# Optimization experiments

Hardware: AMD Instinct MI355X
Metric: run time of the kernel (lower is better)

The kernel has to match this reference:

```python
import jax, jax.numpy as jnp
import numpy as np

# ---- st-moe constants (training-mode routing) ----
EPS = 1e-9
TOP_N = 2
CAP_FACTOR = 1.25      # capacity_factor_train
THRESHOLD = 0.2        # threshold_train (2nd expert)
BAL_COEF = 0.01
Z_COEF = 0.001
MIN_CAP = 4
LN_EPS = 1e-5

B, N, D, E = 4, 2048, 512, 8
H = int(D * 4 * 2 / 3)  # 1365, st-moe default Expert hidden


def _rms_norm(x, gamma):
    # F.normalize(x, dim=-1) * sqrt(d) * gamma
    nrm = jnp.maximum(jnp.linalg.norm(x, axis=-1, keepdims=True), 1e-12)
    return x / nrm * (x.shape[-1] ** 0.5) * gamma


def setup_inputs() -> dict:
    key = jax.random.key(0)
    ks = jax.random.split(key, 6)
    s = 0.02
    return {
        "x": jax.random.normal(ks[0], (B, N, D), jnp.float32),
        "gate_w": jax.random.normal(ks[1], (D, E), jnp.float32) * s,
        "prenorm_g": jnp.ones((D,), jnp.float32),
        "w1": jax.random.normal(ks[2], (E, D, 2 * H), jnp.float32) * s,
        "b1": jnp.zeros((E, 2 * H), jnp.float32),
        "mult_bias": jnp.ones((E, H), jnp.float32),
        "w2": jax.random.normal(ks[3], (E, H, D), jnp.float32) * s,
        "b2": jnp.zeros((E, D), jnp.float32),
        "ln_g": jnp.ones((D,), jnp.float32),
        "ln_b": jnp.zeros((D,), jnp.float32),
    }


def _stmoe_fnn(x, gate_w, prenorm_g, w1, b1, mult_bias, w2, b2, ln_g, ln_b):
    b, n, d = x.shape
    e = gate_w.shape[1]
    cap = max(MIN_CAP, min(n, int(n * CAP_FACTOR / e)))  # static python int

    # SparseMoEBlock: moe(RMSNorm(x)) + x
    xg = _rms_norm(x, prenorm_g)

    # ---- TopNGating ----
    gate_logits = jnp.einsum('bnd,de->bne', xg, gate_w)
    raw_gates = jax.nn.softmax(gate_logits, axis=-1)
    gates, idx = jax.lax.top_k(raw_gates, TOP_N)          # (b,n,k)
    gates = jnp.moveaxis(gates, -1, 0)                    # (k,b,n)
    idx = jnp.moveaxis(idx, -1, 0)                        # (k,b,n)
    one_hot = jax.nn.one_hot(idx, e, dtype=x.dtype)       # (k,b,n,e)

    denom = jnp.maximum(gates.sum(axis=0), EPS)
    gates = gates / denom                                 # normalized top-n scores

    # stochastic routing to non-first experts: prob = min(1, gate/threshold)
    thresh = jnp.array([EPS, THRESHOLD], x.dtype)[:, None, None]
    probs = jax.random.uniform(jax.random.key(42), gates.shape, x.dtype)
    should_route = probs < (gates / jnp.maximum(thresh, EPS))
    should_route = should_route.at[0].set(True)
    mask = one_hot * should_route[..., None].astype(x.dtype)  # (k,b,n,e)

    # exclusive cumsum over sequence -> position within each expert
    mask_cumsum = jnp.cumsum(mask, axis=-2) - mask

    positions, kept_masks = [], []
    prev_count = jnp.zeros((b, 1, e), x.dtype)
    for k in range(TOP_N):  # top_n=2, tiny static loop
        pos_in_expert = (mask_cumsum[k] + prev_count) * mask[k]      # (b,n,e)
        kept = mask[k] * (pos_in_expert < float(cap)).astype(x.dtype)
        prev_count = prev_count + kept.sum(axis=-2, keepdims=True)
        positions.append(pos_in_expert.sum(axis=-1))                 # (b,n)
        kept_masks.append(kept)
    mask = jnp.stack(kept_masks)       # (k,b,n,e) post-capacity
    positions = jnp.stack(positions)   # (k,b,n)

    mask_flat = mask.sum(axis=-1)      # (k,b,n)
    gates = gates * mask_flat

    # safe one-hot: out-of-range (overflow) positions map to all-zeros
    pos_one_hot = jax.nn.one_hot(positions.astype(jnp.int32), cap, dtype=x.dtype)  # (k,b,n,c)
    combine = jnp.einsum('kbn,kbne,kbnc->bnec', gates, one_hot, pos_one_hot)       # (b,n,e,c)

    # straight-through dispatch tensor
    dispatch = (combine > 0).astype(x.dtype) + combine - jax.lax.stop_gradient(combine)

    # ---- dispatch, expert GEGLU FFN, combine ----
    expert_in = jnp.einsum('bnd,bnec->becd', xg, dispatch)                 # (b,e,c,d)
    h = jnp.einsum('becd,edf->becf', expert_in, w1) + b1[None, :, None, :]
    u, g = jnp.split(h, 2, axis=-1)
    act = u * jax.nn.gelu(g, approximate=False) * mult_bias[None, :, None, :]
    expert_out = jnp.einsum('bech,ehd->becd', act, w2) + b2[None, :, None, :]
    moe_out = jnp.einsum('becd,bnec->bnd', expert_out, combine)

    # ---- aux losses (training mode) ----
    density_1 = mask[0].mean(axis=-2)          # (b,e), post-capacity mask (torch in-place view)
    density_proxy = raw_gates.mean(axis=-2)    # (b,e)
    balance_loss = (density_proxy * density_1).mean() * float(e ** 2)
    z = jax.nn.logsumexp(gate_logits, axis=-1)
    router_z_loss = jnp.mean(z * z)
    total_aux = BAL_COEF * balance_loss + Z_COEF * router_z_loss

    # residual, (dropout -> identity for determinism), LayerNorm
    y = moe_out + x
    mu = y.mean(axis=-1, keepdims=True)
    var = jnp.mean((y - mu) ** 2, axis=-1, keepdims=True)
    out = (y - mu) * jax.lax.rsqrt(var + LN_EPS) * ln_g + ln_b
    return out, total_aux


def reference(x, gate_w, prenorm_g, w1, b1, mult_bias, w2, b2, ln_g, ln_b):
    return _stmoe_fnn(x, gate_w, prenorm_g, w1, b1, mult_bias, w2, b2, ln_g, ln_b)
```

## Files before the change

kernel.cpp:

```cpp
#include <hip/hip_runtime.h>
#include <hip/hip_bf16.h>
#include <math.h>

#define BB 4
#define NN 2048
#define DD 512
#define EE 8
#define HH 1365
#define H2 2730
#define CAP 320
#define NT (BB*NN)
#define KP2 1408
#define NW1 2816
#define ME 1280
#define KS1 16
#define KS2 44

typedef __bf16 bf16_t;
typedef __bf16 bf16x4 __attribute__((ext_vector_type(4)));
typedef __bf16 bf16x8 __attribute__((ext_vector_type(8)));
typedef float f32x4 __attribute__((ext_vector_type(4)));

__device__ __forceinline__ float gelu_exact(float x){
    return 0.5f * x * (1.0f + erff(x * 0.70710678118654752f));
}
__device__ __forceinline__ void gl2lds16(const void* g, void* s){
    __builtin_amdgcn_global_load_lds((const __attribute__((address_space(1))) unsigned int*)g,
                                     (__attribute__((address_space(3))) unsigned int*)s,
                                     16, 0, 0);
}
__device__ __forceinline__ unsigned rotl32(unsigned x, int d){ return (x<<d)|(x>>(32-d)); }
__device__ __forceinline__ void tf_round(unsigned &x0, unsigned &x1, int r){
    x0 += x1; x1 = rotl32(x1, r); x1 ^= x0;
}
__device__ float threefry_u01_second(unsigned t){
    const unsigned ks0 = 0u, ks1 = 42u, ks2 = 0x1BD11BDAu ^ 42u;
    unsigned x0 = t, x1 = t + 8192u;
    x0 += ks0; x1 += ks1;
    tf_round(x0,x1,13); tf_round(x0,x1,15); tf_round(x0,x1,26); tf_round(x0,x1,6);
    x0 += ks1; x1 += ks2 + 1u;
    tf_round(x0,x1,17); tf_round(x0,x1,29); tf_round(x0,x1,16); tf_round(x0,x1,24);
    x0 += ks2; x1 += ks0 + 2u;
    tf_round(x0,x1,13); tf_round(x0,x1,15); tf_round(x0,x1,26); tf_round(x0,x1,6);
    x0 += ks0; x1 += ks1 + 3u;
    tf_round(x0,x1,17); tf_round(x0,x1,29); tf_round(x0,x1,16); tf_round(x0,x1,24);
    x0 += ks1; x1 += ks2 + 4u;
    tf_round(x0,x1,13); tf_round(x0,x1,15); tf_round(x0,x1,26); tf_round(x0,x1,6);
    x0 += ks2; x1 += ks0 + 5u;
    unsigned bits = (x1 >> 9) | 0x3f800000u;
    return __uint_as_float(bits) - 1.0f;
}

__global__ void k_gate(const float* __restrict__ x, const float* __restrict__ png,
                       const float* __restrict__ gw, bf16_t* __restrict__ xgb,
                       int* __restrict__ tok_e0, int* __restrict__ tok_e1,
                       float* __restrict__ tok_g0, float* __restrict__ tok_g1,
                       int* __restrict__ tok_c0, int* __restrict__ tok_c1,
                       float* __restrict__ dpPart, float* __restrict__ z2Part){
    if (blockIdx.x == NN){
        xgb[(size_t)NT*DD + threadIdx.x]       = (bf16_t)0.f;
        xgb[(size_t)NT*DD + threadIdx.x + 256] = (bf16_t)0.f;
        return;
    }
    int wave = threadIdx.x >> 6;
    int lane = threadIdx.x & 63;
    int t = blockIdx.x*4 + wave;
    const float* row = x + (size_t)t*DD;
    float xv[8]; float ss = 0.f;
    #pragma unroll
    for (int i=0;i<8;i++){ xv[i] = row[lane + i*64]; ss += xv[i]*xv[i]; }
    #pragma unroll
    for (int off=32; off; off>>=1) ss += __shfl_xor(ss, off);
    float scale = 22.62741699796952f / fmaxf(sqrtf(ss), 1e-12f);
    float acc[EE];
    #pragma unroll
    for (int e=0;e<EE;e++) acc[e]=0.f;
    #pragma unroll
    for (int i=0;i<8;i++){
        int k = lane + i*64;
        float v = xv[i] * scale * png[k];
        xgb[(size_t)t*DD + k] = (bf16_t)v;
        const float* w = gw + k*EE;
        #pragma unroll
        for (int e=0;e<EE;e++) acc[e] = fmaf(v, w[e], acc[e]);
    }
    #pragma unroll
    for (int off=32; off; off>>=1){
        #pragma unroll
        for (int e=0;e<EE;e++) acc[e] += __shfl_down(acc[e], off);
    }
    __shared__ float s_raw[4][EE];
    __shared__ float s_z2[4];
    if (lane==0){
        float mx = acc[0];
        #pragma unroll
        for (int e=1;e<EE;e++) mx = fmaxf(mx, acc[e]);
        float p[EE]; float se=0.f;
        #pragma unroll
        for (int e=0;e<EE;e++){ p[e] = expf(acc[e]-mx); se += p[e]; }
        float inv = 1.f/se;
        #pragma unroll
        for (int e=0;e<EE;e++) p[e] *= inv;
        float z = mx + logf(se);
        int i0=0;
        #pragma unroll
        for (int e=1;e<EE;e++) if (p[e] > p[i0]) i0=e;
        int i1 = (i0==0)?1:0;
        #pragma unroll
        for (int e=0;e<EE;e++){ if (e==i0) continue; if (p[e] > p[i1]) i1=e; }
        float g0=p[i0], g1=p[i1];
        float denom = fmaxf(g0+g1, 1e-9f);
        g0/=denom; g1/=denom;
        float prob = threefry_u01_second((unsigned)t);
        bool route1 = prob < (g1 * 5.0f);
        tok_e0[t] = i0;
        tok_e1[t] = route1 ? i1 : -1;
        tok_g0[t] = g0;
        tok_g1[t] = g1;
        tok_c0[t] = -1;
        tok_c1[t] = -1;
        #pragma unroll
        for (int e=0;e<EE;e++) s_raw[wave][e] = p[e];
        s_z2[wave] = z*z;
    }
    __syncthreads();
    if (threadIdx.x < EE){
        float sum = s_raw[0][threadIdx.x]+s_raw[1][threadIdx.x]+s_raw[2][threadIdx.x]+s_raw[3][threadIdx.x];
        dpPart[threadIdx.x*(size_t)NN + blockIdx.x] = sum;
    }
    if (threadIdx.x == EE) z2Part[blockIdx.x] = s_z2[0]+s_z2[1]+s_z2[2]+s_z2[3];
}

__global__ void k_scan(const int* __restrict__ tok_e0, const int* __restrict__ tok_e1,
                       int* __restrict__ tok_c0, int* __restrict__ tok_c1,
                       int* __restrict__ slot_tok, int* __restrict__ kept0cnt){
    int be = blockIdx.x;
    int b = be >> 3, e = be & 7;
    int tid = threadIdx.x;
    int sbase = (e*BB + b)*CAP;
    for (int i=tid; i<CAP; i+=256) slot_tok[sbase + i] = -1;
    __syncthreads();
    int n0 = tid * 8;
    int base_t = b*NN;
    int m0=0, m1=0;
    for (int i=0;i<8;i++){
        int t = base_t + n0 + i;
        m0 += (tok_e0[t]==e);
        m1 += (tok_e1[t]==e);
    }
    __shared__ int s[256];
    s[tid] = m0 | (m1<<16);
    __syncthreads();
    for (int off=1; off<256; off<<=1){
        int v = 0;
        if (tid >= off) v = s[tid-off];
        __syncthreads();
        if (tid >= off) s[tid] += v;
        __syncthreads();
    }
    int incl = s[tid];
    int total = s[255];
    int p0 = (incl & 0xffff) - m0;
    int p1 = (incl >> 16) - m1;
    int t0 = total & 0xffff;
    int kept0 = min(t0, CAP);
    int c0 = p0, c1 = p1;
    for (int i=0;i<8;i++){
        int n = n0 + i;
        int t = base_t + n;
        if (tok_e0[t]==e){
            int pos = c0++;
            if (pos < CAP){ tok_c0[t] = pos; slot_tok[sbase + pos] = t; }
        }
        if (tok_e1[t]==e){
            int pos = kept0 + c1++;
            if (pos < CAP){ tok_c1[t] = pos; slot_tok[sbase + pos] = t; }
        }
    }
    if (tid==0) kept0cnt[be] = kept0;
}

__global__ void k_aux(const float* __restrict__ dpPart, const float* __restrict__ z2Part,
                      const int* __restrict__ kept0cnt, float* __restrict__ out_aux){
    __shared__ float sdp[32][9];
    __shared__ float sz[256];
    int tid = threadIdx.x;
    float za = 0.f;
    for (int i=tid; i<NN; i+=256) za += z2Part[i];
    sz[tid] = za; __syncthreads();
    for (int off=128; off; off>>=1){ if (tid<off) sz[tid]+=sz[tid+off]; __syncthreads(); }
    int seg = tid >> 3, off8 = tid & 7;
    int b = seg >> 3, e = seg & 7;
    float a = 0.f;
    for (int j=off8; j<512; j+=8) a += dpPart[e*(size_t)NN + b*512 + j];
    sdp[seg][off8] = a;
    __syncthreads();
    if (tid == 0){
        float z2t = sz[0];
        float bal = 0.f;
        for (int sgi=0; sgi<32; sgi++){
            float d = 0.f;
            #pragma unroll
            for (int k=0;k<8;k++) d += sdp[sgi][k];
            float d1 = (float)kept0cnt[sgi] / (float)NN;
            bal += (d / (float)NN) * d1;
        }
        bal = bal / 32.f * 64.f;
        out_aux[0] = 0.01f * bal + 0.001f * (z2t / (float)NT);
    }
}

__global__ void k_w1t(const float* __restrict__ w1, bf16_t* __restrict__ w1t){
    __shared__ float T[32][33];
    int n0 = blockIdx.x * 32;
    int ks = blockIdx.y;
    int e  = blockIdx.z;
    int tx = threadIdx.x & 31;
    int tg = threadIdx.x >> 5;
    int n = n0 + tx;
    #pragma unroll
    for (int i=0;i<4;i++){
        int kk = tg + i*8;
        int k = ks*32 + kk;
        float v = 0.f;
        if (n < KP2){ if (n < HH) v = w1[((size_t)e*DD + k)*H2 + n]; }
        else { int h = n - KP2; if (h < HH) v = w1[((size_t)e*DD + k)*H2 + HH + h]; }
        T[kk][tx] = v;
    }
    __syncthreads();
    int rr = threadIdx.x >> 3, s = threadIdx.x & 7;
    bf16x4 o;
    #pragma unroll
    for (int j=0;j<4;j++) o[j] = (bf16_t)T[s*4+j][rr];
    size_t off = (((size_t)e*KS1 + ks)*NW1 + n0 + rr)*32 + s*4;
    *(bf16x4*)(w1t + off) = o;
}

__global__ void k_w2t(const float* __restrict__ w2, bf16_t* __restrict__ w2t){
    __shared__ float T[32][33];
    int n0 = blockIdx.x * 32;
    int ks = blockIdx.y;
    int e  = blockIdx.z;
    int tx = threadIdx.x & 31;
    int tg = threadIdx.x >> 5;
    #pragma unroll
    for (int i=0;i<4;i++){
        int kk = tg + i*8;
        int k = ks*32 + kk;
        float v = 0.f;
        if (k < HH) v = w2[((size_t)e*HH + k)*DD + n0 + tx];
        T[kk][tx] = v;
    }
    __syncthreads();
    int rr = threadIdx.x >> 3, s = threadIdx.x & 7;
    bf16x4 o;
    #pragma unroll
    for (int j=0;j<4;j++) o[j] = (bf16_t)T[s*4+j][rr];
    size_t off = (((size_t)e*KS2 + ks)*DD + n0 + rr)*32 + s*4;
    *(bf16x4*)(w2t + off) = o;
}

__global__ __launch_bounds__(256,2) void k_ffn1_mfma(
    const bf16_t* __restrict__ xgb, const bf16_t* __restrict__ w1t,
    const float* __restrict__ b1, const float* __restrict__ mbias,
    const int* __restrict__ slot_tok, bf16_t* __restrict__ actb)
{
    int bid = blockIdx.x;
    int e = bid & 7;
    int r = bid >> 3;
    int mblk = r % 10, hb = r / 10;
    int lane = threadIdx.x & 63, wave = threadIdx.x >> 6;
    int quad = lane >> 4, col = lane & 15;
    int wx = wave & 1, wy = wave >> 1;

    __shared__ __align__(16) bf16_t sA[8*512];
    __shared__ __align__(16) bf16_t sB[16*512];

    const bf16_t* gsrc[6];
    bf16_t* sdst[6];
    int gstep[6];
    const size_t w1t_e = (size_t)e*KS1*NW1*32;
    #pragma unroll
    for (int i=0;i<6;i++){
        int id = wave + 4*i;
        if (id < 8){
            int m = mblk*128 + id*16 + col;
            int slot = slot_tok[e*ME + m];
            int row = (slot >= 0) ? slot : NT;
            gsrc[i] = xgb + (size_t)row*DD + quad*8;
            sdst[i] = sA + id*512;
            gstep[i] = 32;
        } else if (id < 16){
            int n = hb*128 + (id-8)*16 + col;
            gsrc[i] = w1t + w1t_e + (size_t)n*32 + quad*8;
            sdst[i] = sB + (id-8)*512;
            gstep[i] = NW1*32;
        } else {
            int n = KP2 + hb*128 + (id-16)*16 + col;
            gsrc[i] = w1t + w1t_e + (size_t)n*32 + quad*8;
            sdst[i] = sB + (id-8)*512;
            gstep[i] = NW1*32;
        }
    }

    f32x4 accU[4][4], accG[4][4];
    #pragma unroll
    for (int mi=0;mi<4;mi++)
        #pragma unroll
        for (int ni=0;ni<4;ni++){
            accU[mi][ni] = (f32x4){0.f,0.f,0.f,0.f};
            accG[mi][ni] = (f32x4){0.f,0.f,0.f,0.f};
        }

    for (int ks=0; ks<KS1; ks++){
        #pragma unroll
        for (int i=0;i<6;i++){ gl2lds16(gsrc[i], sdst[i]); gsrc[i] += gstep[i]; }
        __syncthreads();
        bf16x8 a[4], bu[4], bg[4];
        #pragma unroll
        for (int mi=0;mi<4;mi++) a[mi] = *(const bf16x8*)(sA + (wx*4+mi)*512 + lane*8);
        #pragma unroll
        for (int ni=0;ni<4;ni++){
            bu[ni] = *(const bf16x8*)(sB + (wy*4+ni)*512 + lane*8);
            bg[ni] = *(const bf16x8*)(sB + (8+wy*4+ni)*512 + lane*8);
        }
        #pragma unroll
        for (int mi=0;mi<4;mi++)
            #pragma unroll
            for (int ni=0;ni<4;ni++){
                accU[mi][ni] = __builtin_amdgcn_mfma_f32_16x16x32_bf16(a[mi], bu[ni], accU[mi][ni], 0,0,0);
                accG[mi][ni] = __builtin_amdgcn_mfma_f32_16x16x32_bf16(a[mi], bg[ni], accG[mi][ni], 0,0,0);
            }
        __syncthreads();
    }

    const size_t actb_e = (size_t)e*KS2*ME*32;
    #pragma unroll
    for (int ni=0; ni<4; ni++){
        int h = hb*128 + wy*64 + ni*16 + col;
        bool valid = (h < HH);
        float bu_ = valid ? b1[e*H2 + h] : 0.f;
        float bg_ = valid ? b1[e*H2 + HH + h] : 0.f;
        float mb_ = valid ? mbias[e*HH + h] : 0.f;
        int ks2 = h >> 5, kl = h & 31;
        #pragma unroll
        for (int mi=0; mi<4; mi++){
            int m = mblk*128 + wx*64 + mi*16 + quad*4;
            bf16_t* base = actb + actb_e + ((size_t)ks2*ME + m)*32 + kl;
            #pragma unroll
            for (int rr=0; rr<4; rr++){
                float v = 0.f;
                if (valid){
                    float u = accU[mi][ni][rr] + bu_;
                    float g = accG[mi][ni][rr] + bg_;
                    v = u * gelu_exact(g) * mb_;
                }
                base[rr*32] = (bf16_t)v;
            }
        }
    }
}

__global__ __launch_bounds__(256,4) void k_ffn2_mfma(
    const bf16_t* __restrict__ actb, const bf16_t* __restrict__ w2t,
    const float* __restrict__ b2, float* __restrict__ eo)
{
    int bid = blockIdx.x;
    int e = bid & 7;
    int r = bid >> 3;
    int mblk = r % 10, db = r / 10;
    int lane = threadIdx.x & 63, wave = threadIdx.x >> 6;
    int quad = lane >> 4, col = lane & 15;
    int wx = wave & 1, wy = wave >> 1;

    __shared__ __align__(16) bf16_t sA[8*512];
    __shared__ __align__(16) bf16_t sB[8*512];

    const bf16_t* gsrc[4];
    bf16_t* sdst[4];
    int gstep[4];
    const size_t actb_e = (size_t)e*KS2*ME*32;
    const size_t w2t_e  = (size_t)e*KS2*DD*32;
    #pragma unroll
    for (int i=0;i<4;i++){
        int id = wave + 4*i;
        if (id < 8){
            int m = mblk*128 + id*16 + col;
            gsrc[i] = actb + actb_e + (size_t)m*32 + quad*8;
            sdst[i] = sA + id*512;
            gstep[i] = ME*32;
        } else {
            int d = db*128 + (id-8)*16 + col;
            gsrc[i] = w2t + w2t_e + (size_t)d*32 + quad*8;
            sdst[i] = sB + (id-8)*512;
            gstep[i] = DD*32;
        }
    }

    f32x4 acc[4][4];
    #pragma unroll
    for (int mi=0;mi<4;mi++)
        #pragma unroll
        for (int ni=0;ni<4;ni++) acc[mi][ni] = (f32x4){0.f,0.f,0.f,0.f};

    for (int ks=0; ks<KS2; ks++){
        #pragma unroll
        for (int i=0;i<4;i++){ gl2lds16(gsrc[i], sdst[i]); gsrc[i] += gstep[i]; }
        __syncthreads();
        bf16x8 a[4], bv[4];
        #pragma unroll
        for (int mi=0;mi<4;mi++) a[mi] = *(const bf16x8*)(sA + (wx*4+mi)*512 + lane*8);
        #pragma unroll
        for (int ni=0;ni<4;ni++) bv[ni] = *(const bf16x8*)(sB + (wy*4+ni)*512 + lane*8);
        #pragma unroll
        for (int mi=0;mi<4;mi++)
            #pragma unroll
            for (int ni=0;ni<4;ni++)
                acc[mi][ni] = __builtin_amdgcn_mfma_f32_16x16x32_bf16(a[mi], bv[ni], acc[mi][ni], 0,0,0);
        __syncthreads();
    }

    #pragma unroll
    for (int ni=0; ni<4; ni++){
        int d = db*128 + wy*64 + ni*16 + col;
        float bb = b2[e*DD + d];
        #pragma unroll
        for (int mi=0; mi<4; mi++){
            int m = mblk*128 + wx*64 + mi*16 + quad*4;
            #pragma unroll
            for (int rr=0; rr<4; rr++)
                eo[((size_t)e*ME + m + rr)*DD + d] = acc[mi][ni][rr] + bb;
        }
    }
}

__global__ void k_combine(const float* __restrict__ x, const float* __restrict__ eo,
        const int* __restrict__ tok_e0, const int* __restrict__ tok_e1,
        const int* __restrict__ tok_c0, const int* __restrict__ tok_c1,
        const float* __restrict__ tok_g0, const float* __restrict__ tok_g1,
        const float* __restrict__ ln_g, const float* __restrict__ ln_b,
        float* __restrict__ out){
    int t = blockIdx.x;
    int b = t / NN;
    int e0 = tok_e0[t], c0 = tok_c0[t];
    int e1 = tok_e1[t], c1 = tok_c1[t];
    float g0 = tok_g0[t], g1 = tok_g1[t];
    const float* r0 = (c0>=0) ? eo + ((size_t)(e0*ME + b*CAP + c0))*DD : nullptr;
    const float* r1 = (e1>=0 && c1>=0) ? eo + ((size_t)(e1*ME + b*CAP + c1))*DD : nullptr;
    float y[2]; float s=0.f, s2=0.f;
    #pragma unroll
    for (int i=0;i<2;i++){
        int d = threadIdx.x + i*256;
        float v = x[(size_t)t*DD + d];
        if (r0) v = fmaf(g0, r0[d], v);
        if (r1) v = fmaf(g1, r1[d], v);
        y[i]=v; s+=v; s2+=v*v;
    }
    __shared__ float rs[4], rs2[4];
    #pragma unroll
    for (int off=32; off; off>>=1){ s+=__shfl_down(s,off); s2+=__shfl_down(s2,off); }
    if ((threadIdx.x&63)==0){ rs[threadIdx.x>>6]=s; rs2[threadIdx.x>>6]=s2; }
    __syncthreads();
    float mu  = (rs[0]+rs[1]+rs[2]+rs[3]) * (1.0f/512.0f);
    float var = (rs2[0]+rs2[1]+rs2[2]+rs2[3]) * (1.0f/512.0f) - mu*mu;
    float inv = rsqrtf(var + 1e-5f);
    #pragma unroll
    for (int i=0;i<2;i++){
        int d = threadIdx.x + i*256;
        out[(size_t)t*DD + d] = (y[i]-mu)*inv*ln_g[d] + ln_b[d];
    }
}

extern "C" void kernel_launch(void* const* d_in, const int* in_sizes, int n_in,
                              void* d_out, int out_size, void* d_ws, size_t ws_size,
                              hipStream_t stream) {
    const float* x         = (const float*)d_in[0];
    const float* gate_w    = (const float*)d_in[1];
    const float* prenorm_g = (const float*)d_in[2];
    const float* w1        = (const float*)d_in[3];
    const float* b1        = (const float*)d_in[4];
    const float* mult_bias = (const float*)d_in[5];
    const float* w2        = (const float*)d_in[6];
    const float* b2        = (const float*)d_in[7];
    const float* ln_g      = (const float*)d_in[8];
    const float* ln_b      = (const float*)d_in[9];
    float* out = (float*)d_out;

    char* p = (char*)d_ws;
    bf16_t* xgb = (bf16_t*)p; p += (size_t)(NT+1)*DD*2;
    bf16_t* w1t = (bf16_t*)p; p += (size_t)EE*KS1*NW1*32*2;
    bf16_t* w2t = (bf16_t*)p; p += (size_t)EE*KS2*DD*32*2;
    bf16_t* actb = (bf16_t*)p; p += (size_t)EE*KS2*ME*32*2;
    float* eo  = (float*)p; p += (size_t)EE*ME*DD*4;
    int* slot_tok = (int*)p; p += EE*BB*CAP*4;
    int* tok_e0 = (int*)p; p += NT*4;
    int* tok_e1 = (int*)p; p += NT*4;
    int* tok_c0 = (int*)p; p += NT*4;
    int* tok_c1 = (int*)p; p += NT*4;
    float* tok_g0 = (float*)p; p += NT*4;
    float* tok_g1 = (float*)p; p += NT*4;
    float* dpPart = (float*)p; p += EE*NN*4;
    float* z2Part = (float*)p; p += NN*4;
    int* kept0 = (int*)p; p += BB*EE*4;

    k_w1t<<<dim3(NW1/32, KS1, EE), 256, 0, stream>>>(w1, w1t);
    k_w2t<<<dim3(DD/32, KS2, EE), 256, 0, stream>>>(w2, w2t);
    k_gate<<<NN+1, 256, 0, stream>>>(x, prenorm_g, gate_w, xgb,
                                     tok_e0, tok_e1, tok_g0, tok_g1,
                                     tok_c0, tok_c1, dpPart, z2Part);
    k_scan<<<BB*EE, 256, 0, stream>>>(tok_e0, tok_e1, tok_c0, tok_c1, slot_tok, kept0);
    k_aux<<<1, 256, 0, stream>>>(dpPart, z2Part, kept0, out + (size_t)NT*DD);
    k_ffn1_mfma<<<EE*10*11, 256, 0, stream>>>(xgb, w1t, b1, mult_bias, slot_tok, actb);
    k_ffn2_mfma<<<EE*10*4, 256, 0, stream>>>(actb, w2t, b2, eo);
    k_combine<<<NT, 256, 0, stream>>>(x, eo, tok_e0, tok_e1, tok_c0, tok_c1,
                                      tok_g0, tok_g1, ln_g, ln_b, out);
}
```

Baseline: 272.6 us.

## Fuse prep kernels, split-K FFN2 with bf16 partials, retile FFN1, vectorize combine

Merges the weight transposes and gating into a single prep launch and folds the aux-loss reduction into the scan kernel using a last-block atomic counter. FFN1 is retiled to 512-thread blocks covering 256 rows so the weight tile is reused across more tokens. FFN2 is split along K into two halves that write bf16 partial outputs, and the combine kernel sums them, adds the bias and uses float4 loads. This aims to cut launch overhead, raise GEMM parallelism and reduce expert-output traffic, at the cost of lower output precision and an extra partial buffer.

Result: no change. 269.1 us (-1.3%).

```diff
diff --git a/kernel.cpp b/kernel.cpp
--- a/kernel.cpp
+++ b/kernel.cpp
@@ -51,89 +51,152 @@
     return __uint_as_float(bits) - 1.0f;
 }
 
-__global__ void k_gate(const float* __restrict__ x, const float* __restrict__ png,
-                       const float* __restrict__ gw, bf16_t* __restrict__ xgb,
+#define PREP_GATE  2048
+#define PREP_W1    (PREP_GATE+1)
+#define PREP_W2    (PREP_W1+11264)
+__global__ void k_prep(const float* __restrict__ x, const float* __restrict__ png,
+                       const float* __restrict__ gw,
+                       const float* __restrict__ w1, const float* __restrict__ w2,
+                       bf16_t* __restrict__ xgb, bf16_t* __restrict__ w1t, bf16_t* __restrict__ w2t,
                        int* __restrict__ tok_e0, int* __restrict__ tok_e1,
                        float* __restrict__ tok_g0, float* __restrict__ tok_g1,
                        int* __restrict__ tok_c0, int* __restrict__ tok_c1,
-                       float* __restrict__ dpPart, float* __restrict__ z2Part){
-    if (blockIdx.x == NN){
+                       float* __restrict__ dpPart, float* __restrict__ z2Part,
+                       unsigned* __restrict__ scanCnt){
+    __shared__ float T[32][33];
+    __shared__ float s_raw[4][EE];
+    __shared__ float s_z2[4];
+    int bid = blockIdx.x;
+    if (bid < PREP_GATE){
+        int wave = threadIdx.x >> 6;
+        int lane = threadIdx.x & 63;
+        int t = bid*4 + wave;
+        const float* row = x + (size_t)t*DD;
+        float xv[8]; float ss = 0.f;
+        #pragma unroll
+        for (int i=0;i<8;i++){ xv[i] = row[lane + i*64]; ss += xv[i]*xv[i]; }
+        #pragma unroll
+        for (int off=32; off; off>>=1) ss += __shfl_xor(ss, off);
+        float scale = 22.62741699796952f / fmaxf(sqrtf(ss), 1e-12f);
+        float acc[EE];
+        #pragma unroll
+        for (int e=0;e<EE;e++) acc[e]=0.f;
+        #pragma unroll
+        for (int i=0;i<8;i++){
+            int k = lane + i*64;
+            float v = xv[i] * scale * png[k];
+            xgb[(size_t)t*DD + k] = (bf16_t)v;
+            const float* w = gw + k*EE;
+            #pragma unroll
+            for (int e=0;e<EE;e++) acc[e] = fmaf(v, w[e], acc[e]);
+        }
+        #pragma unroll
+        for (int off=32; off; off>>=1){
+            #pragma unroll
+            for (int e=0;e<EE;e++) acc[e] += __shfl_down(acc[e], off);
+        }
+        if (lane==0){
+            float mx = acc[0];
+            #pragma unroll
+            for (int e=1;e<EE;e++) mx = fmaxf(mx, acc[e]);
+            float p[EE]; float se=0.f;
+            #pragma unroll
+            for (int e=0;e<EE;e++){ p[e] = expf(acc[e]-mx); se += p[e]; }
+            float inv = 1.f/se;
+            #pragma unroll
+            for (int e=0;e<EE;e++) p[e] *= inv;
+            float z = mx + logf(se);
+            int i0=0;
+            #pragma unroll
+            for (int e=1;e<EE;e++) if (p[e] > p[i0]) i0=e;
+            int i1 = (i0==0)?1:0;
+            #pragma unroll
+            for (int e=0;e<EE;e++){ if (e==i0) continue; if (p[e] > p[i1]) i1=e; }
+            float g0=p[i0], g1=p[i1];
+            float denom = fmaxf(g0+g1, 1e-9f);
+            g0/=denom; g1/=denom;
+            float prob = threefry_u01_second((unsigned)t);
+            bool route1 = prob < (g1 * 5.0f);
+            tok_e0[t] = i0;
+            tok_e1[t] = route1 ? i1 : -1;
+            tok_g0[t] = g0;
+            tok_g1[t] = g1;
+            tok_c0[t] = -1;
+            tok_c1[t] = -1;
+            #pragma unroll
+            for (int e=0;e<EE;e++) s_raw[wave][e] = p[e];
+            s_z2[wave] = z*z;
+        }
+        __syncthreads();
+        if (threadIdx.x < EE){
+            float sum = s_raw[0][threadIdx.x]+s_raw[1][threadIdx.x]+s_raw[2][threadIdx.x]+s_raw[3][threadIdx.x];
+            dpPart[threadIdx.x*(size_t)NN + bid] = sum;
+        }
+        if (threadIdx.x == EE) z2Part[bid] = s_z2[0]+s_z2[1]+s_z2[2]+s_z2[3];
+    } else if (bid == PREP_GATE){
         xgb[(size_t)NT*DD + threadIdx.x]       = (bf16_t)0.f;
         xgb[(size_t)NT*DD + threadIdx.x + 256] = (bf16_t)0.f;
-        return;
-    }
-    int wave = threadIdx.x >> 6;
-    int lane = threadIdx.x & 63;
-    int t = blockIdx.x*4 + wave;
-    const float* row = x + (size_t)t*DD;
-    float xv[8]; float ss = 0.f;
-    #pragma unroll
-    for (int i=0;i<8;i++){ xv[i] = row[lane + i*64]; ss += xv[i]*xv[i]; }
-    #pragma unroll
-    for (int off=32; off; off>>=1) ss += __shfl_xor(ss, off);
-    float scale = 22.62741699796952f / fmaxf(sqrtf(ss), 1e-12f);
-    float acc[EE];
-    #pragma unroll
-    for (int e=0;e<EE;e++) acc[e]=0.f;
-    #pragma unroll
-    for (int i=0;i<8;i++){
-        int k = lane + i*64;
-        float v = xv[i] * scale * png[k];
-        xgb[(size_t)t*DD + k] = (bf16_t)v;
-        const float* w = gw + k*EE;
-        #pragma unroll
-        for (int e=0;e<EE;e++) acc[e] = fmaf(v, w[e], acc[e]);
-    }
-    #pragma unroll
-    for (int off=32; off; off>>=1){
-        #pragma unroll
-        for (int e=0;e<EE;e++) acc[e] += __shfl_down(acc[e], off);
-    }
-    __shared__ float s_raw[4][EE];
-    __shared__ float s_z2[4];
-    if (lane==0){
-        float mx = acc[0];
-        #pragma unroll
-        for (int e=1;e<EE;e++) mx = fmaxf(mx, acc[e]);
-        float p[EE]; float se=0.f;
-        #pragma unroll
-        for (int e=0;e<EE;e++){ p[e] = expf(acc[e]-mx); se += p[e]; }
-        float inv = 1.f/se;
-        #pragma unroll
-        for (int e=0;e<EE;e++) p[e] *= inv;
-        float z = mx + logf(se);
-        int i0=0;
-        #pragma unroll
-        for (int e=1;e<EE;e++) if (p[e] > p[i0]) i0=e;
-        int i1 = (i0==0)?1:0;
-        #pragma unroll
-        for (int e=0;e<EE;e++){ if (e==i0) continue; if (p[e] > p[i1]) i1=e; }
-        float g0=p[i0], g1=p[i1];
-        float denom = fmaxf(g0+g1, 1e-9f);
-        g0/=denom; g1/=denom;
-        float prob = threefry_u01_second((unsigned)t);
-        bool route1 = prob < (g1 * 5.0f);
-        tok_e0[t] = i0;
-        tok_e1[t] = route1 ? i1 : -1;
-        tok_g0[t] = g0;
-        tok_g1[t] = g1;
-        tok_c0[t] = -1;
-        tok_c1[t] = -1;
-        #pragma unroll
-        for (int e=0;e<EE;e++) s_raw[wave][e] = p[e];
-        s_z2[wave] = z*z;
-    }
-    __syncthreads();
-    if (threadIdx.x < EE){
-        float sum = s_raw[0][threadIdx.x]+s_raw[1][threadIdx.x]+s_raw[2][threadIdx.x]+s_raw[3][threadIdx.x];
-        dpPart[threadIdx.x*(size_t)NN + blockIdx.x] = sum;
-    }
-    if (threadIdx.x == EE) z2Part[blockIdx.x] = s_z2[0]+s_z2[1]+s_z2[2]+s_z2[3];
+        if (threadIdx.x == 0) scanCnt[0] = 0u;
+    } else if (bid < PREP_W2){
+        int f = bid - PREP_W1;
+        int n32 = f % 88;
+        int ks  = (f / 88) % 16;
+        int e   = f / 1408;
+        int n0 = n32 * 32;
+        int tx = threadIdx.x & 31;
+        int tg = threadIdx.x >> 5;
+        int n = n0 + tx;
+        #pragma unroll
+        for (int i=0;i<4;i++){
+            int kk = tg + i*8;
+            int k = ks*32 + kk;
+            float v = 0.f;
+            if (n < KP2){ if (n < HH) v = w1[((size_t)e*DD + k)*H2 + n]; }
+            else { int h = n - KP2; if (h < HH) v = w1[((size_t)e*DD + k)*H2 + HH + h]; }
+            T[kk][tx] = v;
+        }
+        __syncthreads();
+        int rr = threadIdx.x >> 3, s = threadIdx.x & 7;
+        bf16x4 o;
+        #pragma unroll
+        for (int j=0;j<4;j++) o[j] = (bf16_t)T[s*4+j][rr];
+        size_t off = (((size_t)e*KS1 + ks)*NW1 + n0 + rr)*32 + s*4;
+        *(bf16x4*)(w1t + off) = o;
+    } else {
+        int f = bid - PREP_W2;
+        int d32 = f % 16;
+        int ks  = (f / 16) % 44;
+        int e   = f / 704;
+        int n0 = d32 * 32;
+        int tx = threadIdx.x & 31;
+        int tg = threadIdx.x >> 5;
+        #pragma unroll
+        for (int i=0;i<4;i++){
+            int kk = tg + i*8;
+            int k = ks*32 + kk;
+            float v = 0.f;
+            if (k < HH) v = w2[((size_t)e*HH + k)*DD + n0 + tx];
+            T[kk][tx] = v;
+        }
+        __syncthreads();
+        int rr = threadIdx.x >> 3, s = threadIdx.x & 7;
+        bf16x4 o;
+        #pragma unroll
+        for (int j=0;j<4;j++) o[j] = (bf16_t)T[s*4+j][rr];
+        size_t off = (((size_t)e*KS2 + ks)*DD + n0 + rr)*32 + s*4;
+        *(bf16x4*)(w2t + off) = o;
+    }
 }
 
 __global__ void k_scan(const int* __restrict__ tok_e0, const int* __restrict__ tok_e1,
                        int* __restrict__ tok_c0, int* __restrict__ tok_c1,
-                       int* __restrict__ slot_tok, int* __restrict__ kept0cnt){
+                       int* __restrict__ slot_tok, int* __restrict__ kept0cnt,
+                       const float* __restrict__ dpPart, const float* __restrict__ z2Part,
+                       unsigned* __restrict__ scanCnt, float* __restrict__ out_aux){
+    __shared__ int s[256];
+    __shared__ float sdp[32][9];
+    __shared__ float sz[256];
+    __shared__ bool s_last;
     int be = blockIdx.x;
     int b = be >> 3, e = be & 7;
     int tid = threadIdx.x;
@@ -148,7 +211,6 @@
         m0 += (tok_e0[t]==e);
         m1 += (tok_e1[t]==e);
     }
-    __shared__ int s[256];
     s[tid] = m0 | (m1<<16);
     __syncthreads();
     for (int off=1; off<256; off<<=1){
@@ -178,21 +240,23 @@
         }
     }
     if (tid==0) kept0cnt[be] = kept0;
-}
-
-__global__ void k_aux(const float* __restrict__ dpPart, const float* __restrict__ z2Part,
-                      const int* __restrict__ kept0cnt, float* __restrict__ out_aux){
-    __shared__ float sdp[32][9];
-    __shared__ float sz[256];
-    int tid = threadIdx.x;
+    __threadfence();
+    __syncthreads();
+    if (tid==0){
+        unsigned old = atomicAdd(scanCnt, 1u);
+        s_last = (old == (unsigned)(BB*EE - 1));
+    }
+    __syncthreads();
+    if (!s_last) return;
+    __threadfence();
     float za = 0.f;
     for (int i=tid; i<NN; i+=256) za += z2Part[i];
     sz[tid] = za; __syncthreads();
     for (int off=128; off; off>>=1){ if (tid<off) sz[tid]+=sz[tid+off]; __syncthreads(); }
     int seg = tid >> 3, off8 = tid & 7;
-    int b = seg >> 3, e = seg & 7;
+    int bb2 = seg >> 3, ee2 = seg & 7;
     float a = 0.f;
-    for (int j=off8; j<512; j+=8) a += dpPart[e*(size_t)NN + b*512 + j];
+    for (int j=off8; j<512; j+=8) a += dpPart[ee2*(size_t)NN + bb2*512 + j];
     sdp[seg][off8] = a;
     __syncthreads();
     if (tid == 0){
@@ -210,57 +274,7 @@
     }
 }
 
-__global__ void k_w1t(const float* __restrict__ w1, bf16_t* __restrict__ w1t){
-    __shared__ float T[32][33];
-    int n0 = blockIdx.x * 32;
-    int ks = blockIdx.y;
-    int e  = blockIdx.z;
-    int tx = threadIdx.x & 31;
-    int tg = threadIdx.x >> 5;
-    int n = n0 + tx;
-    #pragma unroll
-    for (int i=0;i<4;i++){
-        int kk = tg + i*8;
-        int k = ks*32 + kk;
-        float v = 0.f;
-        if (n < KP2){ if (n < HH) v = w1[((size_t)e*DD + k)*H2 + n]; }
-        else { int h = n - KP2; if (h < HH) v = w1[((size_t)e*DD + k)*H2 + HH + h]; }
-        T[kk][tx] = v;
-    }
-    __syncthreads();
-    int rr = threadIdx.x >> 3, s = threadIdx.x & 7;
-    bf16x4 o;
-    #pragma unroll
-    for (int j=0;j<4;j++) o[j] = (bf16_t)T[s*4+j][rr];
-    size_t off = (((size_t)e*KS1 + ks)*NW1 + n0 + rr)*32 + s*4;
-    *(bf16x4*)(w1t + off) = o;
-}
-
-__global__ void k_w2t(const float* __restrict__ w2, bf16_t* __restrict__ w2t){
-    __shared__ float T[32][33];
-    int n0 = blockIdx.x * 32;
-    int ks = blockIdx.y;
-    int e  = blockIdx.z;
-    int tx = threadIdx.x & 31;
-    int tg = threadIdx.x >> 5;
-    #pragma unroll
-    for (int i=0;i<4;i++){
-        int kk = tg + i*8;
-        int k = ks*32 + kk;
-        float v = 0.f;
-        if (k < HH) v = w2[((size_t)e*HH + k)*DD + n0 + tx];
-        T[kk][tx] = v;
-    }
-    __syncthreads();
-    int rr = threadIdx.x >> 3, s = threadIdx.x & 7;
-    bf16x4 o;
-    #pragma unroll
-    for (int j=0;j<4;j++) o[j] = (bf16_t)T[s*4+j][rr];
-    size_t off = (((size_t)e*KS2 + ks)*DD + n0 + rr)*32 + s*4;
-    *(bf16x4*)(w2t + off) = o;
-}
-
-__global__ __launch_bounds__(256,2) void k_ffn1_mfma(
+__global__ __launch_bounds__(512,2) void k_ffn1_mfma(
     const bf16_t* __restrict__ xgb, const bf16_t* __restrict__ w1t,
     const float* __restrict__ b1, const float* __restrict__ mbias,
     const int* __restrict__ slot_tok, bf16_t* __restrict__ actb)
@@ -268,37 +282,38 @@
     int bid = blockIdx.x;
     int e = bid & 7;
     int r = bid >> 3;
-    int mblk = r % 10, hb = r / 10;
+    int mblk = r % 5, hb = r / 5;
     int lane = threadIdx.x & 63, wave = threadIdx.x >> 6;
     int quad = lane >> 4, col = lane & 15;
-    int wx = wave & 1, wy = wave >> 1;
-
-    __shared__ __align__(16) bf16_t sA[8*512];
-    __shared__ __align__(16) bf16_t sB[16*512];
-
-    const bf16_t* gsrc[6];
-    bf16_t* sdst[6];
-    int gstep[6];
+    int wm = wave & 3, wn = wave >> 2;
+
+    __shared__ __align__(16) bf16_t sA[16*512];
+    __shared__ __align__(16) bf16_t sBu[8*512];
+    __shared__ __align__(16) bf16_t sBg[8*512];
+
+    const bf16_t* gsrc[4];
+    bf16_t* sdst[4];
+    int gstep[4];
     const size_t w1t_e = (size_t)e*KS1*NW1*32;
     #pragma unroll
-    for (int i=0;i<6;i++){
-        int id = wave + 4*i;
-        if (id < 8){
-            int m = mblk*128 + id*16 + col;
+    for (int i=0;i<4;i++){
+        int id = wave + 8*i;
+        if (id < 16){
+            int m = mblk*256 + id*16 + col;
             int slot = slot_tok[e*ME + m];
             int row = (slot >= 0) ? slot : NT;
             gsrc[i] = xgb + (size_t)row*DD + quad*8;
             sdst[i] = sA + id*512;
             gstep[i] = 32;
-        } else if (id < 16){
-            int n = hb*128 + (id-8)*16 + col;
+        } else if (id < 24){
+            int n = hb*128 + (id-16)*16 + col;
             gsrc[i] = w1t + w1t_e + (size_t)n*32 + quad*8;
-            sdst[i] = sB + (id-8)*512;
+            sdst[i] = sBu + (id-16)*512;
             gstep[i] = NW1*32;
         } else {
-            int n = KP2 + hb*128 + (id-16)*16 + col;
+            int n = KP2 + hb*128 + (id-24)*16 + col;
             gsrc[i] = w1t + w1t_e + (size_t)n*32 + quad*8;
-            sdst[i] = sB + (id-8)*512;
+            sdst[i] = sBg + (id-24)*512;
             gstep[i] = NW1*32;
         }
     }
@@ -314,15 +329,15 @@
 
     for (int ks=0; ks<KS1; ks++){
         #pragma unroll
-        for (int i=0;i<6;i++){ gl2lds16(gsrc[i], sdst[i]); gsrc[i] += gstep[i]; }
+        for (int i=0;i<4;i++){ gl2lds16(gsrc[i], sdst[i]); gsrc[i] += gstep[i]; }
         __syncthreads();
         bf16x8 a[4], bu[4], bg[4];
         #pragma unroll
-        for (int mi=0;mi<4;mi++) a[mi] = *(const bf16x8*)(sA + (wx*4+mi)*512 + lane*8);
+        for (int mi=0;mi<4;mi++) a[mi] = *(const bf16x8*)(sA + (wm*4+mi)*512 + lane*8);
         #pragma unroll
         for (int ni=0;ni<4;ni++){
-            bu[ni] = *(const bf16x8*)(sB + (wy*4+ni)*512 + lane*8);
-            bg[ni] = *(const bf16x8*)(sB + (8+wy*4+ni)*512 + lane*8);
+            bu[ni] = *(const bf16x8*)(sBu + (wn*4+ni)*512 + lane*8);
+            bg[ni] = *(const bf16x8*)(sBg + (wn*4+ni)*512 + lane*8);
         }
         #pragma unroll
         for (int mi=0;mi<4;mi++)
@@ -337,7 +352,7 @@
     const size_t actb_e = (size_t)e*KS2*ME*32;
     #pragma unroll
     for (int ni=0; ni<4; ni++){
-        int h = hb*128 + wy*64 + ni*16 + col;
+        int h = hb*128 + wn*64 + ni*16 + col;
         bool valid = (h < HH);
         float bu_ = valid ? b1[e*H2 + h] : 0.f;
         float bg_ = valid ? b1[e*H2 + HH + h] : 0.f;
@@ -345,7 +360,7 @@
         int ks2 = h >> 5, kl = h & 31;
         #pragma unroll
         for (int mi=0; mi<4; mi++){
-            int m = mblk*128 + wx*64 + mi*16 + quad*4;
+            int m = mblk*256 + wm*64 + mi*16 + quad*4;
             bf16_t* base = actb + actb_e + ((size_t)ks2*ME + m)*32 + kl;
             #pragma unroll
             for (int rr=0; rr<4; rr++){
@@ -363,12 +378,14 @@
 
 __global__ __launch_bounds__(256,4) void k_ffn2_mfma(
     const bf16_t* __restrict__ actb, const bf16_t* __restrict__ w2t,
-    const float* __restrict__ b2, float* __restrict__ eo)
+    bf16_t* __restrict__ eoA, bf16_t* __restrict__ eoB)
 {
     int bid = blockIdx.x;
     int e = bid & 7;
     int r = bid >> 3;
-    int mblk = r % 10, db = r / 10;
+    int mblk = r % 10;
+    int q = r / 10;
+    int db = q & 3, kh = q >> 2;
     int lane = threadIdx.x & 63, wave = threadIdx.x >> 6;
     int quad = lane >> 4, col = lane & 15;
     int wx = wave & 1, wy = wave >> 1;
@@ -379,8 +396,8 @@
     const bf16_t* gsrc[4];
     bf16_t* sdst[4];
     int gstep[4];
-    const size_t actb_e = (size_t)e*KS2*ME*32;
-    const size_t w2t_e  = (size_t)e*KS2*DD*32;
+    const size_t actb_e = (size_t)e*KS2*ME*32 + (size_t)(kh*22)*ME*32;
+    const size_t w2t_e  = (size_t)e*KS2*DD*32 + (size_t)(kh*22)*DD*32;
     #pragma unroll
     for (int i=0;i<4;i++){
         int id = wave + 4*i;
@@ -403,7 +420,7 @@
         #pragma unroll
         for (int ni=0;ni<4;ni++) acc[mi][ni] = (f32x4){0.f,0.f,0.f,0.f};
 
-    for (int ks=0; ks<KS2; ks++){
+    for (int ks=0; ks<22; ks++){
         #pragma unroll
         for (int i=0;i<4;i++){ gl2lds16(gsrc[i], sdst[i]); gsrc[i] += gstep[i]; }
         __syncthreads();
@@ -420,55 +437,75 @@
         __syncthreads();
     }
 
+    bf16_t* eop = kh ? eoB : eoA;
     #pragma unroll
     for (int ni=0; ni<4; ni++){
         int d = db*128 + wy*64 + ni*16 + col;
-        float bb = b2[e*DD + d];
         #pragma unroll
         for (int mi=0; mi<4; mi++){
             int m = mblk*128 + wx*64 + mi*16 + quad*4;
             #pragma unroll
             for (int rr=0; rr<4; rr++)
-                eo[((size_t)e*ME + m + rr)*DD + d] = acc[mi][ni][rr] + bb;
-        }
-    }
-}
-
-__global__ void k_combine(const float* __restrict__ x, const float* __restrict__ eo,
+                eop[((size_t)e*ME + m + rr)*DD + d] = (bf16_t)acc[mi][ni][rr];
+        }
+    }
+}
+
+__global__ void k_combine(const float* __restrict__ x,
+        const bf16_t* __restrict__ eoA, const bf16_t* __restrict__ eoB,
         const int* __restrict__ tok_e0, const int* __restrict__ tok_e1,
         const int* __restrict__ tok_c0, const int* __restrict__ tok_c1,
         const float* __restrict__ tok_g0, const float* __restrict__ tok_g1,
+        const float* __restrict__ b2,
         const float* __restrict__ ln_g, const float* __restrict__ ln_b,
         float* __restrict__ out){
     int t = blockIdx.x;
     int b = t / NN;
+    int tid = threadIdx.x;
+    int i4 = tid*4;
     int e0 = tok_e0[t], c0 = tok_c0[t];
     int e1 = tok_e1[t], c1 = tok_c1[t];
     float g0 = tok_g0[t], g1 = tok_g1[t];
-    const float* r0 = (c0>=0) ? eo + ((size_t)(e0*ME + b*CAP + c0))*DD : nullptr;
-    const float* r1 = (e1>=0 && c1>=0) ? eo + ((size_t)(e1*ME + b*CAP + c1))*DD : nullptr;
-    float y[2]; float s=0.f, s2=0.f;
-    #pragma unroll
-    for (int i=0;i<2;i++){
-        int d = threadIdx.x + i*256;
-        float v = x[(size_t)t*DD + d];
-        if (r0) v = fmaf(g0, r0[d], v);
-        if (r1) v = fmaf(g1, r1[d], v);
-        y[i]=v; s+=v; s2+=v*v;
-    }
-    __shared__ float rs[4], rs2[4];
-    #pragma unroll
-    for (int off=32; off; off>>=1){ s+=__shfl_down(s,off); s2+=__shfl_down(s2,off); }
-    if ((threadIdx.x&63)==0){ rs[threadIdx.x>>6]=s; rs2[threadIdx.x>>6]=s2; }
+    float4 xv = *(const float4*)(x + (size_t)t*DD + i4);
+    float v[4] = {xv.x, xv.y, xv.z, xv.w};
+    if (c0 >= 0){
+        size_t idx = ((size_t)(e0*ME + b*CAP + c0))*DD + i4;
+        bf16x4 pa = *(const bf16x4*)(eoA + idx);
+        bf16x4 pb = *(const bf16x4*)(eoB + idx);
+        float4 bb = *(const float4*)(b2 + e0*DD + i4);
+        v[0] += g0 * ((float)pa[0] + (float)pb[0] + bb.x);
+        v[1] += g0 * ((float)pa[1] + (float)pb[1] + bb.y);
+        v[2] += g0 * ((float)pa[2] + (float)pb[2] + bb.z);
+        v[3] += g0 * ((float)pa[3] + (float)pb[3] + bb.w);
+    }
+    if (e1 >= 0 && c1 >= 0){
+        size_t idx = ((size_t)(e1*ME + b*CAP + c1))*DD + i4;
+        bf16x4 pa = *(const bf16x4*)(eoA + idx);
+        bf16x4 pb = *(const bf16x4*)(eoB + idx);
+        float4 bb = *(const float4*)(b2 + e1*DD + i4);
+        v[0] += g1 * ((float)pa[0] + (float)pb[0] + bb.x);
+        v[1] += g1 * ((float)pa[1] + (float)pb[1] + bb.y);
+        v[2] += g1 * ((float)pa[2] + (float)pb[2] + bb.z);
+        v[3] += g1 * ((float)pa[3] + (float)pb[3] + bb.w);
+    }
+    float s = v[0]+v[1]+v[2]+v[3];
+    float s2 = v[0]*v[0]+v[1]*v[1]+v[2]*v[2]+v[3]*v[3];
+    __shared__ float rs[2], rs2[2];
+    #pragma unroll
+    for (int off=32; off; off>>=1){ s += __shfl_down(s,off); s2 += __shfl_down(s2,off); }
+    if ((tid&63)==0){ rs[tid>>6]=s; rs2[tid>>6]=s2; }
     __syncthreads();
-    float mu  = (rs[0]+rs[1]+rs[2]+rs[3]) * (1.0f/512.0f);
-    float var = (rs2[0]+rs2[1]+rs2[2]+rs2[3]) * (1.0f/512.0f) - mu*mu;
+    float mu  = (rs[0]+rs[1]) * (1.0f/512.0f);
+    float var = (rs2[0]+rs2[1]) * (1.0f/512.0f) - mu*mu;
     float inv = rsqrtf(var + 1e-5f);
-    #pragma unroll
-    for (int i=0;i<2;i++){
-        int d = threadIdx.x + i*256;
-        out[(size_t)t*DD + d] = (y[i]-mu)*inv*ln_g[d] + ln_b[d];
-    }
+    float4 gv = *(const float4*)(ln_g + i4);
+    float4 bv = *(const float4*)(ln_b + i4);
+    float4 o;
+    o.x = (v[0]-mu)*inv*gv.x + bv.x;
+    o.y = (v[1]-mu)*inv*gv.y + bv.y;
+    o.z = (v[2]-mu)*inv*gv.z + bv.z;
+    o.w = (v[3]-mu)*inv*gv.w + bv.w;
+    *(float4*)(out + (size_t)t*DD + i4) = o;
 }
 
 extern "C" void kernel_launch(void* const* d_in, const int* in_sizes, int n_in,
@@ -491,7 +528,8 @@
     bf16_t* w1t = (bf16_t*)p; p += (size_t)EE*KS1*NW1*32*2;
     bf16_t* w2t = (bf16_t*)p; p += (size_t)EE*KS2*DD*32*2;
     bf16_t* actb = (bf16_t*)p; p += (size_t)EE*KS2*ME*32*2;
-    float* eo  = (float*)p; p += (size_t)EE*ME*DD*4;
+    bf16_t* eoA = (bf16_t*)p; p += (size_t)EE*ME*DD*2;
+    bf16_t* eoB = (bf16_t*)p; p += (size_t)EE*ME*DD*2;
     int* slot_tok = (int*)p; p += EE*BB*CAP*4;
     int* tok_e0 = (int*)p; p += NT*4;
     int* tok_e1 = (int*)p; p += NT*4;
@@ -502,16 +540,16 @@
     float* dpPart = (float*)p; p += EE*NN*4;
     float* z2Part = (float*)p; p += NN*4;
     int* kept0 = (int*)p; p += BB*EE*4;
-
-    k_w1t<<<dim3(NW1/32, KS1, EE), 256, 0, stream>>>(w1, w1t);
-    k_w2t<<<dim3(DD/32, KS2, EE), 256, 0, stream>>>(w2, w2t);
-    k_gate<<<NN+1, 256, 0, stream>>>(x, prenorm_g, gate_w, xgb,
-                                     tok_e0, tok_e1, tok_g0, tok_g1,
-                                     tok_c0, tok_c1, dpPart, z2Part);
-    k_scan<<<BB*EE, 256, 0, stream>>>(tok_e0, tok_e1, tok_c0, tok_c1, slot_tok, kept0);
-    k_aux<<<1, 256, 0, stream>>>(dpPart, z2Part, kept0, out + (size_t)NT*DD);
-    k_ffn1_mfma<<<EE*10*11, 256, 0, stream>>>(xgb, w1t, b1, mult_bias, slot_tok, actb);
-    k_ffn2_mfma<<<EE*10*4, 256, 0, stream>>>(actb, w2t, b2, eo);
-    k_combine<<<NT, 256, 0, stream>>>(x, eo, tok_e0, tok_e1, tok_c0, tok_c1,
-                                      tok_g0, tok_g1, ln_g, ln_b, out);
-}
+    unsigned* scanCnt = (unsigned*)p; p += 4;
+
+    k_prep<<<PREP_W2 + 5632, 256, 0, stream>>>(x, prenorm_g, gate_w, w1, w2,
+                                               xgb, w1t, w2t,
+                                               tok_e0, tok_e1, tok_g0, tok_g1,
+                                               tok_c0, tok_c1, dpPart, z2Part, scanCnt);
+    k_scan<<<BB*EE, 256, 0, stream>>>(tok_e0, tok_e1, tok_c0, tok_c1, slot_tok, kept0,
+                                      dpPart, z2Part, scanCnt, out + (size_t)NT*DD);
+    k_ffn1_mfma<<<EE*5*11, 512, 0, stream>>>(xgb, w1t, b1, mult_bias, slot_tok, actb);
+    k_ffn2_mfma<<<EE*10*4*2, 256, 0, stream>>>(actb, w2t, eoA, eoB);
+    k_combine<<<NT, 128, 0, stream>>>(x, eoA, eoB, tok_e0, tok_e1, tok_c0, tok_c1,
+                                      tok_g0, tok_g1, b2, ln_g, ln_b, out);
+}
```
